# Performance work log

Hardware: AMD Instinct MI355X
Metric: run time of the kernel (lower is better)

Reference implementation:

```python
import jax, jax.numpy as jnp
import numpy as np

N_NODES = 50000
N_EDGES = 500000
NODE_D = 128
EDGE_D = 128
IN_D = EDGE_D + 2 * NODE_D  # 384


def setup_inputs() -> dict:
    key = jax.random.key(0)
    k1, k2, k3, k4, k5, k6 = jax.random.split(key, 6)
    nodes = jax.random.normal(k1, (N_NODES, NODE_D), dtype=jnp.float32)
    edges = jax.random.normal(k2, (N_EDGES, EDGE_D), dtype=jnp.float32)
    receivers = jax.random.randint(k3, (N_EDGES,), 0, N_NODES, dtype=jnp.int64)
    senders = jax.random.randint(k4, (N_EDGES,), 0, N_NODES, dtype=jnp.int64)
    # Linear(IN_D, EDGE_D): W is [out, in] like torch, b is [out]
    W = jax.random.normal(k5, (EDGE_D, IN_D), dtype=jnp.float32) * (1.0 / np.sqrt(IN_D))
    b = jax.random.normal(k6, (EDGE_D,), dtype=jnp.float32) * 0.01
    return {"nodes": nodes, "edges": edges, "receivers": receivers,
            "senders": senders, "W": W, "b": b}


def reference(nodes, edges, receivers, senders, W, b):
    # gather receiver / sender node features to edges, concat with edge feats
    recv = jnp.take(nodes, receivers, axis=0)   # [E, NODE_D]
    send = jnp.take(nodes, senders, axis=0)     # [E, NODE_D]
    collected = jnp.concatenate([edges, recv, send], axis=-1)  # [E, IN_D]
    updated_edges = collected @ W.T + b          # [E, EDGE_D]
    return updated_edges
```

## Files before the change

### kernel.cpp

```cpp
#include <hip/hip_runtime.h>


#define NODE_D 128
#define EDGE_D 128
#define IN_D   384
#define OUT_D  128
#define BM 128
#define BN 128
#define BK 32
#define SA 40
#define NCHUNK 12

typedef __attribute__((ext_vector_type(8))) short bf16x8;
typedef __attribute__((ext_vector_type(4))) float floatx4;

static __device__ __forceinline__ unsigned int pack_bf16x2(float lo, float hi) {
    unsigned int a = __builtin_bit_cast(unsigned int, lo);
    unsigned int b = __builtin_bit_cast(unsigned int, hi);
    a += 0x7fffu + ((a >> 16) & 1u);
    b += 0x7fffu + ((b >> 16) & 1u);
    return (a >> 16) | (b & 0xffff0000u);
}

__global__ __launch_bounds__(256, 2)
void edgeblock_gemm(const float* __restrict__ nodes,
                    const float* __restrict__ edges,
                    const int*   __restrict__ recv,
                    const int*   __restrict__ send,
                    const float* __restrict__ W,
                    const float* __restrict__ bias,
                    float*       __restrict__ out,
                    int E)
{
    __shared__ __align__(16) unsigned short As[2][BM * SA];
    __shared__ __align__(16) unsigned short Bs[2][BN * SA];

    const int tid   = threadIdx.x;
    const int lane8 = tid & 7;
    const int h     = tid >> 3;
    const int wave  = tid >> 6;
    const int lane  = tid & 63;
    const int quad  = lane >> 4;
    const int l16   = lane & 15;
    const int wm    = (wave >> 1) * 64;
    const int wn    = (wave & 1) * 64;
    const long e0   = (long)blockIdx.x * BM;

    const float* baseE[4];
    const float* baseR[4];
    const float* baseS[4];
    #pragma unroll
    for (int i = 0; i < 4; ++i) {
        long e = e0 + h + 32 * i;
        if (e > (long)E - 1) e = (long)E - 1;
        baseE[i] = edges + e * (long)EDGE_D;
        baseR[i] = nodes + (long)recv[e] * NODE_D;
        baseS[i] = nodes + (long)send[e] * NODE_D;
    }

    float4 va[4], vb[4];

    auto loadChunk = [&](int c) {
        const int col = (c & 3) * 32;
        #pragma unroll
        for (int i = 0; i < 4; ++i) {
            const float* src = (c < 4) ? baseE[i] : (c < 8) ? baseR[i] : baseS[i];
            va[i] = *(const float4*)(src + col + lane8 * 4);
            vb[i] = *(const float4*)(W + (long)(h + 32 * i) * IN_D + c * 32 + lane8 * 4);
        }
    };
    auto writeChunk = [&](int buf) {
        #pragma unroll
        for (int i = 0; i < 4; ++i) {
            uint2 pa, pb;
            pa.x = pack_bf16x2(va[i].x, va[i].y);
            pa.y = pack_bf16x2(va[i].z, va[i].w);
            pb.x = pack_bf16x2(vb[i].x, vb[i].y);
            pb.y = pack_bf16x2(vb[i].z, vb[i].w);
            *(uint2*)&As[buf][(h + 32 * i) * SA + lane8 * 4] = pa;
            *(uint2*)&Bs[buf][(h + 32 * i) * SA + lane8 * 4] = pb;
        }
    };

    floatx4 acc[4][4] = {};

    loadChunk(0);
    writeChunk(0);
    __syncthreads();

    #pragma unroll
    for (int c = 0; c < NCHUNK; ++c) {
        if (c + 1 < NCHUNK) loadChunk(c + 1);
        const int buf = c & 1;

        bf16x8 af[4], bfr[4];
        #pragma unroll
        for (int mi = 0; mi < 4; ++mi)
            af[mi] = *(const bf16x8*)&As[buf][(wm + mi * 16 + l16) * SA + quad * 8];
        #pragma unroll
        for (int ni = 0; ni < 4; ++ni)
            bfr[ni] = *(const bf16x8*)&Bs[buf][(wn + ni * 16 + l16) * SA + quad * 8];
        #pragma unroll
        for (int mi = 0; mi < 4; ++mi)
            #pragma unroll
            for (int ni = 0; ni < 4; ++ni)
                acc[mi][ni] = __builtin_amdgcn_mfma_f32_16x16x32_bf16(
                    af[mi], bfr[ni], acc[mi][ni], 0, 0, 0);

        if (c + 1 < NCHUNK) writeChunk((c + 1) & 1);
        __syncthreads();
    }

    float bv[4];
    #pragma unroll
    for (int ni = 0; ni < 4; ++ni) bv[ni] = bias[wn + ni * 16 + l16];

    #pragma unroll
    for (int mi = 0; mi < 4; ++mi) {
        #pragma unroll
        for (int r = 0; r < 4; ++r) {
            long row = e0 + wm + mi * 16 + quad * 4 + r;
            if (row < (long)E) {
                float* orow = out + row * (long)OUT_D + wn + l16;
                #pragma unroll
                for (int ni = 0; ni < 4; ++ni)
                    orow[ni * 16] = acc[mi][ni][r] + bv[ni];
            }
        }
    }
}

extern "C" void kernel_launch(void* const* d_in, const int* in_sizes, int n_in,
                              void* d_out, int out_size, void* d_ws, size_t ws_size,
                              hipStream_t stream) {
    const float* nodes = (const float*)d_in[0];
    const float* edges = (const float*)d_in[1];
    const int*   recv  = (const int*)d_in[2];
    const int*   send  = (const int*)d_in[3];
    const float* W     = (const float*)d_in[4];
    const float* bias  = (const float*)d_in[5];
    float* out = (float*)d_out;

    const int E = in_sizes[2];
    const int grid = (E + BM - 1) / BM;

    edgeblock_gemm<<<grid, 256, 0, stream>>>(nodes, edges, recv, send, W, bias, out, E);
}
```

Baseline: 530.5 us.

## Pre-convert nodes and W to bf16, gather node rows directly into LDS

Adds a pre-pass that converts the node table and W to bf16 in workspace, so each gathered node row is half as many bytes. The main kernel then gathers receiver/sender rows into swizzled LDS with global_load_lds, bypassing registers. It also reads W fragments straight from global/L2 into registers instead of staging them in LDS. The aim is to cut gather bandwidth and LDS traffic, at the cost of two extra launches and a read/write pass over the node table each call. The old kernel is kept as a fallback when workspace is too small.

```diff
diff --git a/kernel.cpp b/kernel.cpp
--- a/kernel.cpp
+++ b/kernel.cpp
@@ -1,18 +1,16 @@
 #include <hip/hip_runtime.h>
 
 
-#define NODE_D 128
-#define EDGE_D 128
-#define IN_D   384
-#define OUT_D  128
 #define BM 128
-#define BN 128
-#define BK 32
-#define SA 40
-#define NCHUNK 12
+#define NCH 12
 
 typedef __attribute__((ext_vector_type(8))) short bf16x8;
 typedef __attribute__((ext_vector_type(4))) float floatx4;
+typedef __attribute__((ext_vector_type(4))) unsigned int uint4v;
+
+#define GLOAD_LDS16(g, l) __builtin_amdgcn_global_load_lds(                    \
+    (const __attribute__((address_space(1))) unsigned int*)(g),                \
+    (__attribute__((address_space(3))) unsigned int*)(l), 16, 0, 0)
 
 static __device__ __forceinline__ unsigned int pack_bf16x2(float lo, float hi) {
     unsigned int a = __builtin_bit_cast(unsigned int, lo);
@@ -22,51 +20,173 @@
     return (a >> 16) | (b & 0xffff0000u);
 }
 
+__global__ void cvt_bf16(const float* __restrict__ src, unsigned int* __restrict__ dst, int n4) {
+    int i = blockIdx.x * blockDim.x + threadIdx.x;
+    if (i < n4) {
+        float4 v = ((const float4*)src)[i];
+        uint2 p;
+        p.x = pack_bf16x2(v.x, v.y);
+        p.y = pack_bf16x2(v.z, v.w);
+        ((uint2*)dst)[i] = p;
+    }
+}
+
 __global__ __launch_bounds__(256, 2)
-void edgeblock_gemm(const float* __restrict__ nodes,
-                    const float* __restrict__ edges,
-                    const int*   __restrict__ recv,
-                    const int*   __restrict__ send,
-                    const float* __restrict__ W,
-                    const float* __restrict__ bias,
-                    float*       __restrict__ out,
-                    int E)
+void edge_gemm_v2(const float* __restrict__ edges,
+                  const int*   __restrict__ recv,
+                  const int*   __restrict__ send,
+                  const unsigned short* __restrict__ nodes_bf,
+                  const unsigned short* __restrict__ w_bf,
+                  const float* __restrict__ bias,
+                  float*       __restrict__ out,
+                  int E)
 {
-    __shared__ __align__(16) unsigned short As[2][BM * SA];
-    __shared__ __align__(16) unsigned short Bs[2][BN * SA];
-
-    const int tid   = threadIdx.x;
-    const int lane8 = tid & 7;
-    const int h     = tid >> 3;
-    const int wave  = tid >> 6;
-    const int lane  = tid & 63;
-    const int quad  = lane >> 4;
-    const int l16   = lane & 15;
-    const int wm    = (wave >> 1) * 64;
-    const int wn    = (wave & 1) * 64;
-    const long e0   = (long)blockIdx.x * BM;
-
-    const float* baseE[4];
-    const float* baseR[4];
-    const float* baseS[4];
+    __shared__ __align__(16) unsigned short As[2][BM * 32];
+
+    const int tid  = threadIdx.x;
+    const int wave = tid >> 6, lane = tid & 63;
+    const int quad = lane >> 4, l16 = lane & 15;
+    const int wm = (wave >> 1) * 64, wn = (wave & 1) * 64;
+    const long e0 = (long)blockIdx.x * BM;
+
+    const int rl   = lane >> 2;
+    const int sblk = (lane & 3) ^ ((lane >> 3) & 3);
+    long er0 = e0 + wave * 32 + rl;      if (er0 > (long)E - 1) er0 = (long)E - 1;
+    long er1 = e0 + wave * 32 + 16 + rl; if (er1 > (long)E - 1) er1 = (long)E - 1;
+    const unsigned short* gR0 = nodes_bf + (long)recv[er0] * 128 + sblk * 8;
+    const unsigned short* gR1 = nodes_bf + (long)recv[er1] * 128 + sblk * 8;
+    const unsigned short* gS0 = nodes_bf + (long)send[er0] * 128 + sblk * 8;
+    const unsigned short* gS1 = nodes_bf + (long)send[er1] * 128 + sblk * 8;
+
+    const int erow = tid >> 1;
+    long ee = e0 + erow; if (ee > (long)E - 1) ee = (long)E - 1;
+    const float* eptr = edges + ee * 128L;
+    const int swzE = (erow >> 1) & 3;
+    const int b0 = (tid & 1) * 2;
+    const int s0 = b0 ^ swzE, s1 = (b0 + 1) ^ swzE;
+
+    floatx4 acc[4][4] = {};
+    float4 ev[4];
+
+    auto edge_issue = [&](int c) {
+        const float* p = eptr + c * 32;
+        ev[0] = *(const float4*)(p + s0 * 8);
+        ev[1] = *(const float4*)(p + s0 * 8 + 4);
+        ev[2] = *(const float4*)(p + s1 * 8);
+        ev[3] = *(const float4*)(p + s1 * 8 + 4);
+    };
+    auto edge_write = [&](int buf) {
+        uint4v w0, w1;
+        w0.x = pack_bf16x2(ev[0].x, ev[0].y); w0.y = pack_bf16x2(ev[0].z, ev[0].w);
+        w0.z = pack_bf16x2(ev[1].x, ev[1].y); w0.w = pack_bf16x2(ev[1].z, ev[1].w);
+        w1.x = pack_bf16x2(ev[2].x, ev[2].y); w1.y = pack_bf16x2(ev[2].z, ev[2].w);
+        w1.z = pack_bf16x2(ev[3].x, ev[3].y); w1.w = pack_bf16x2(ev[3].z, ev[3].w);
+        *(uint4v*)&As[buf][erow * 32 + b0 * 8]       = w0;
+        *(uint4v*)&As[buf][erow * 32 + (b0 + 1) * 8] = w1;
+    };
+    auto node_issue = [&](int c, int buf) {
+        const int off = (c & 3) * 32;
+        const unsigned short* g0 = (c < 8) ? gR0 : gS0;
+        const unsigned short* g1 = (c < 8) ? gR1 : gS1;
+        GLOAD_LDS16(g0 + off, &As[buf][(wave * 2 + 0) * 512]);
+        GLOAD_LDS16(g1 + off, &As[buf][(wave * 2 + 1) * 512]);
+    };
+
+    bf16x8 bcur[4], bnext[4];
+    auto loadB = [&](int c, bf16x8* b) {
+        #pragma unroll
+        for (int ni = 0; ni < 4; ++ni)
+            b[ni] = *(const bf16x8*)(w_bf + (long)(wn + ni * 16 + l16) * 384 + c * 32 + quad * 8);
+    };
+
+    edge_issue(0);
+    loadB(0, bcur);
+    edge_write(0);
+    __syncthreads();
+
+    #pragma unroll
+    for (int c = 0; c < NCH; ++c) {
+        const int buf = c & 1;
+        if (c + 1 < NCH) {
+            if (c + 1 < 4) edge_issue(c + 1);
+            else           node_issue(c + 1, buf ^ 1);
+            loadB(c + 1, bnext);
+        }
+        bf16x8 af[4];
+        #pragma unroll
+        for (int mi = 0; mi < 4; ++mi)
+            af[mi] = *(const bf16x8*)&As[buf][(wm + mi * 16 + l16) * 32 +
+                                             ((quad ^ ((l16 >> 1) & 3)) * 8)];
+        #pragma unroll
+        for (int mi = 0; mi < 4; ++mi)
+            #pragma unroll
+            for (int ni = 0; ni < 4; ++ni)
+                acc[mi][ni] = __builtin_amdgcn_mfma_f32_16x16x32_bf16(
+                    af[mi], bcur[ni], acc[mi][ni], 0, 0, 0);
+        if (c + 1 < NCH) {
+            if (c + 1 < 4) edge_write(buf ^ 1);
+            #pragma unroll
+            for (int ni = 0; ni < 4; ++ni) bcur[ni] = bnext[ni];
+        }
+        __syncthreads();
+    }
+
+    float bv[4];
+    #pragma unroll
+    for (int ni = 0; ni < 4; ++ni) bv[ni] = bias[wn + ni * 16 + l16];
+    #pragma unroll
+    for (int mi = 0; mi < 4; ++mi) {
+        #pragma unroll
+        for (int r = 0; r < 4; ++r) {
+            long row = e0 + wm + mi * 16 + quad * 4 + r;
+            if (row < (long)E) {
+                float* orow = out + row * 128L + wn + l16;
+                #pragma unroll
+                for (int ni = 0; ni < 4; ++ni)
+                    orow[ni * 16] = acc[mi][ni][r] + bv[ni];
+            }
+        }
+    }
+}
+
+#define SA 40
+typedef __attribute__((ext_vector_type(8))) short bf16x8f;
+
+__global__ __launch_bounds__(256, 2)
+void edgeblock_gemm_fb(const float* __restrict__ nodes,
+                       const float* __restrict__ edges,
+                       const int*   __restrict__ recv,
+                       const int*   __restrict__ send,
+                       const float* __restrict__ W,
+                       const float* __restrict__ bias,
+                       float*       __restrict__ out,
+                       int E)
+{
+    __shared__ __align__(16) unsigned short Asf[2][BM * SA];
+    __shared__ __align__(16) unsigned short Bsf[2][BM * SA];
+    const int tid = threadIdx.x;
+    const int lane8 = tid & 7, h = tid >> 3;
+    const int wave = tid >> 6, lane = tid & 63;
+    const int quad = lane >> 4, l16 = lane & 15;
+    const int wm = (wave >> 1) * 64, wn = (wave & 1) * 64;
+    const long e0 = (long)blockIdx.x * BM;
+    const float *baseE[4], *baseR[4], *baseS[4];
     #pragma unroll
     for (int i = 0; i < 4; ++i) {
         long e = e0 + h + 32 * i;
         if (e > (long)E - 1) e = (long)E - 1;
-        baseE[i] = edges + e * (long)EDGE_D;
-        baseR[i] = nodes + (long)recv[e] * NODE_D;
-        baseS[i] = nodes + (long)send[e] * NODE_D;
-    }
-
+        baseE[i] = edges + e * 128L;
+        baseR[i] = nodes + (long)recv[e] * 128;
+        baseS[i] = nodes + (long)send[e] * 128;
+    }
     float4 va[4], vb[4];
-
     auto loadChunk = [&](int c) {
         const int col = (c & 3) * 32;
         #pragma unroll
         for (int i = 0; i < 4; ++i) {
             const float* src = (c < 4) ? baseE[i] : (c < 8) ? baseR[i] : baseS[i];
             va[i] = *(const float4*)(src + col + lane8 * 4);
-            vb[i] = *(const float4*)(W + (long)(h + 32 * i) * IN_D + c * 32 + lane8 * 4);
+            vb[i] = *(const float4*)(W + (long)(h + 32 * i) * 384 + c * 32 + lane8 * 4);
         }
     };
     auto writeChunk = [&](int buf) {
@@ -77,57 +197,47 @@
             pa.y = pack_bf16x2(va[i].z, va[i].w);
             pb.x = pack_bf16x2(vb[i].x, vb[i].y);
             pb.y = pack_bf16x2(vb[i].z, vb[i].w);
-            *(uint2*)&As[buf][(h + 32 * i) * SA + lane8 * 4] = pa;
-            *(uint2*)&Bs[buf][(h + 32 * i) * SA + lane8 * 4] = pb;
-        }
-    };
-
+            *(uint2*)&Asf[buf][(h + 32 * i) * SA + lane8 * 4] = pa;
+            *(uint2*)&Bsf[buf][(h + 32 * i) * SA + lane8 * 4] = pb;
+        }
+    };
     floatx4 acc[4][4] = {};
-
-    loadChunk(0);
-    writeChunk(0);
-    __syncthreads();
-
-    #pragma unroll
-    for (int c = 0; c < NCHUNK; ++c) {
-        if (c + 1 < NCHUNK) loadChunk(c + 1);
+    loadChunk(0); writeChunk(0); __syncthreads();
+    #pragma unroll
+    for (int c = 0; c < NCH; ++c) {
+        if (c + 1 < NCH) loadChunk(c + 1);
         const int buf = c & 1;
-
-        bf16x8 af[4], bfr[4];
-        #pragma unroll
-        for (int mi = 0; mi < 4; ++mi)
-            af[mi] = *(const bf16x8*)&As[buf][(wm + mi * 16 + l16) * SA + quad * 8];
+        bf16x8f af[4], bfr[4];
+        #pragma unroll
+        for (int mi = 0; mi < 4; ++mi)
+            af[mi] = *(const bf16x8f*)&Asf[buf][(wm + mi * 16 + l16) * SA + quad * 8];
         #pragma unroll
         for (int ni = 0; ni < 4; ++ni)
-            bfr[ni] = *(const bf16x8*)&Bs[buf][(wn + ni * 16 + l16) * SA + quad * 8];
+            bfr[ni] = *(const bf16x8f*)&Bsf[buf][(wn + ni * 16 + l16) * SA + quad * 8];
         #pragma unroll
         for (int mi = 0; mi < 4; ++mi)
             #pragma unroll
             for (int ni = 0; ni < 4; ++ni)
                 acc[mi][ni] = __builtin_amdgcn_mfma_f32_16x16x32_bf16(
                     af[mi], bfr[ni], acc[mi][ni], 0, 0, 0);
-
-        if (c + 1 < NCHUNK) writeChunk((c + 1) & 1);
+        if (c + 1 < NCH) writeChunk((c + 1) & 1);
         __syncthreads();
     }
-
     float bv[4];
     #pragma unroll
     for (int ni = 0; ni < 4; ++ni) bv[ni] = bias[wn + ni * 16 + l16];
-
-    #pragma unroll
-    for (int mi = 0; mi < 4; ++mi) {
+    #pragma unroll
+    for (int mi = 0; mi < 4; ++mi)
         #pragma unroll
         for (int r = 0; r < 4; ++r) {
             long row = e0 + wm + mi * 16 + quad * 4 + r;
             if (row < (long)E) {
-                float* orow = out + row * (long)OUT_D + wn + l16;
+                float* orow = out + row * 128L + wn + l16;
                 #pragma unroll
                 for (int ni = 0; ni < 4; ++ni)
                     orow[ni * 16] = acc[mi][ni][r] + bv[ni];
             }
         }
-    }
 }
 
 extern "C" void kernel_launch(void* const* d_in, const int* in_sizes, int n_in,
@@ -144,5 +254,20 @@
     const int E = in_sizes[2];
     const int grid = (E + BM - 1) / BM;
 
-    edgeblock_gemm<<<grid, 256, 0, stream>>>(nodes, edges, recv, send, W, bias, out, E);
-}
+    const size_t nodes_bytes = (size_t)in_sizes[0] * 2;
+    const size_t need = nodes_bytes + (size_t)in_sizes[4] * 2;
+    if (ws_size < need) {
+        edgeblock_gemm_fb<<<grid, 256, 0, stream>>>(nodes, edges, recv, send, W, bias, out, E);
+        return;
+    }
+
+    unsigned short* nodes_bf = (unsigned short*)d_ws;
+    unsigned short* w_bf     = (unsigned short*)((char*)d_ws + nodes_bytes);
+
+    const int n4n = in_sizes[0] / 4;
+    cvt_bf16<<<(n4n + 255) / 256, 256, 0, stream>>>(nodes, (unsigned int*)nodes_bf, n4n);
+    const int n4w = in_sizes[4] / 4;
+    cvt_bf16<<<(n4w + 255) / 256, 256, 0, stream>>>(W, (unsigned int*)w_bf, n4w);
+
+    edge_gemm_v2<<<grid, 256, 0, stream>>>(edges, recv, send, nodes_bf, w_bf, bias, out, E);
+}
```

After: 524.5 us. About the same (-1.1%).
